# Kernel tuning notes

Hardware: AMD Instinct MI355X
Metric: run time of the kernel (lower is better)

The kernel has to match this reference:

```python
import jax, jax.numpy as jnp
import numpy as np

CH = 256
CQK = CH // 8
B, H, W = 4, 64, 64


def setup_inputs() -> dict:
    key = jax.random.key(0)
    ks = jax.random.split(key, 8)
    s_qk = 1.0 / np.sqrt(CH)  # MSR init for 1x1 conv: std = 1/sqrt(fan_in)
    x = jax.random.normal(ks[0], (B, CH, H, W), dtype=jnp.float32)
    Wq = jax.random.normal(ks[1], (CQK, CH), dtype=jnp.float32) * s_qk
    bq = jnp.zeros((CQK,), dtype=jnp.float32)
    Wk = jax.random.normal(ks[2], (CQK, CH), dtype=jnp.float32) * s_qk
    bk = jnp.zeros((CQK,), dtype=jnp.float32)
    Wv = jax.random.normal(ks[3], (CH, CH), dtype=jnp.float32) * s_qk
    bv = jnp.zeros((CH,), dtype=jnp.float32)
    # NOTE: module inits gamma=0; use a nonzero value so the attention branch is active
    gamma = jnp.float32(0.5) * jnp.ones((1,), dtype=jnp.float32)
    return {"x": x, "Wq": Wq, "bq": bq, "Wk": Wk, "bk": bk, "Wv": Wv, "bv": bv, "gamma": gamma}


def reference(x, Wq, bq, Wk, bk, Wv, bv, gamma):
    b, c, h, w = x.shape
    n = h * w
    xf = x.reshape(b, c, n)  # [B, C, N]
    # 1x1 convs are per-pixel channel projections
    q = jnp.einsum('oc,bcn->bon', Wq, xf) + bq[:, None]  # [B, C/8, N]
    k = jnp.einsum('oc,bcn->bon', Wk, xf) + bk[:, None]  # [B, C/8, N]
    v = jnp.einsum('oc,bcn->bon', Wv, xf) + bv[:, None]  # [B, C, N]
    # scores[b, i, j] = q[:, i] . k[:, j]  (no scaling, as in source)
    att = jax.nn.softmax(jnp.einsum('bci,bcj->bij', q, k), axis=-1)  # [B, N, N]
    out = jnp.einsum('bcj,bij->bci', v, att).reshape(b, c, h, w)
    return x + gamma[0] * out
```

## Files before the change

kernel.cpp:

```cpp
#include <hip/hip_runtime.h>
#include <hip/hip_bf16.h>

typedef unsigned short u16;
typedef __attribute__((ext_vector_type(8))) __bf16 bf16x8;
typedef __attribute__((ext_vector_type(8))) short s16x8;
typedef __attribute__((ext_vector_type(4))) float f32x4;
typedef __attribute__((ext_vector_type(16))) float f32x16;

#define MFMA16(a, b, c) __builtin_amdgcn_mfma_f32_16x16x32_bf16((a), (b), (c), 0, 0, 0)
#define MFMA32(a, b, c) __builtin_amdgcn_mfma_f32_32x32x16_bf16((a), (b), (c), 0, 0, 0)

#define BN 4
#define CH 256
#define CQK 32
#define NPIX 4096

__device__ __forceinline__ u16 f2bf(float f) {
    __hip_bfloat16 h = __float2bfloat16(f);
    return *reinterpret_cast<u16*>(&h);
}

__device__ __forceinline__ f32x16 zero16() {
    f32x16 z;
#pragma unroll
    for (int i = 0; i < 16; ++i) z[i] = 0.f;
    return z;
}

__device__ __forceinline__ int perm16(int k) {
    return (k & 3) | ((k & 4) << 1) | ((k & 8) >> 1);
}

__global__ void k_transpose(const float* __restrict__ x, u16* __restrict__ xt) {
    __shared__ float xs[64][65];
    int n0 = blockIdx.x * 64, c0 = blockIdx.y * 64, b = blockIdx.z;
    int t = threadIdx.x;
    const float* xp = x + ((size_t)(b * CH + c0)) * NPIX + n0;
#pragma unroll
    for (int it = 0; it < 16; ++it) {
        int idx = it * 256 + t;
        int cc = idx >> 6, nn = idx & 63;
        xs[cc][nn] = xp[(size_t)cc * NPIX + nn];
    }
    __syncthreads();
    u16* op = xt + ((size_t)(b * NPIX + n0)) * CH + c0;
#pragma unroll
    for (int it = 0; it < 16; ++it) {
        int idx = it * 256 + t;
        int nn = idx >> 6, cc = idx & 63;
        op[(size_t)nn * CH + cc] = f2bf(xs[cc][nn]);
    }
}

__global__ void k_wcvt(const float* __restrict__ Wq, const float* __restrict__ Wk,
                       const float* __restrict__ Wv, u16* __restrict__ Wbf) {
    int idx = blockIdx.x * 256 + threadIdx.x;
    int o = idx >> 8, c = idx & 255;
    float v;
    if (o < 32) v = Wq[o * 256 + c];
    else if (o < 64) v = Wk[(o - 32) * 256 + c];
    else v = Wv[(o - 64) * 256 + c];
    Wbf[idx] = f2bf(v);
}

__launch_bounds__(256, 1)
__global__ void k_proj(const u16* __restrict__ Wbf, const u16* __restrict__ xt,
                       const float* __restrict__ bq, const float* __restrict__ bk,
                       const float* __restrict__ bv,
                       u16* __restrict__ qb, u16* __restrict__ kb, u16* __restrict__ vb) {
    int b = blockIdx.y, n0 = blockIdx.x * 64;
    int t = threadIdx.x, w = t >> 6, l = t & 63;
    int lr = l & 15, lg = l >> 4;

    f32x4 acc[5][4];
#pragma unroll
    for (int s = 0; s < 5; ++s)
#pragma unroll
        for (int u = 0; u < 4; ++u) acc[s][u] = f32x4{0.f, 0.f, 0.f, 0.f};

    const u16* xtb = xt + ((size_t)(b * NPIX + n0)) * CH;

#pragma unroll
    for (int kk = 0; kk < 8; ++kk) {
        int kof = kk * 32 + lg * 8;
        bf16x8 af[5], bfr[4];
#pragma unroll
        for (int s = 0; s < 5; ++s) {
            int o = w * 16 + s * 64 + lr;
            af[s] = *reinterpret_cast<const bf16x8*>(Wbf + (size_t)o * 256 + kof);
        }
#pragma unroll
        for (int u = 0; u < 4; ++u) {
            int n = u * 16 + lr;
            bfr[u] = *reinterpret_cast<const bf16x8*>(xtb + (size_t)n * CH + kof);
        }
#pragma unroll
        for (int s = 0; s < 5; ++s)
#pragma unroll
            for (int u = 0; u < 4; ++u) acc[s][u] = MFMA16(af[s], bfr[u], acc[s][u]);
    }

    int lrp = perm16(lr);
#pragma unroll
    for (int s = 0; s < 5; ++s) {
        int o0 = w * 16 + s * 64;
#pragma unroll
        for (int r = 0; r < 4; ++r) {
            int o = o0 + lg * 4 + r;
            float bias = (o < 32) ? bq[o] : (o < 64) ? bk[o - 32] : bv[o - 64];
#pragma unroll
            for (int u = 0; u < 4; ++u) {
                float val = acc[s][u][r] + bias;
                u16 h = f2bf(val);
                if (o < 32) qb[((size_t)b * NPIX + n0 + u * 16 + lr) * CQK + o] = h;
                else if (o < 64) kb[((size_t)b * NPIX + n0 + u * 16 + lr) * CQK + (o - 32)] = h;
                else vb[((size_t)(b * CH + (o - 64))) * NPIX + n0 + u * 16 + lrp] = h;
            }
        }
    }
}

template <int NCHUNK>
__launch_bounds__(256, 2)
__global__ void k_attn2(const u16* __restrict__ qb, const u16* __restrict__ kb,
                        const u16* __restrict__ vb, const float* __restrict__ x,
                        const float* __restrict__ gamma,
                        float* __restrict__ pacc, float* __restrict__ plsum,
                        float* __restrict__ out) {
    constexpr int JCH = NPIX / NCHUNK;
    constexpr int NT = JCH / 32;
    int it = blockIdx.x, s = blockIdx.y, b = blockIdx.z;
    int t = threadIdx.x, w = t >> 6, l = t & 63;
    int lr = l & 31, hi = l >> 5;
    int i0 = it * 128;
    int j0 = s * JCH;

    __shared__ u16 vlds[2][256][40];
    __shared__ float lsl[128];

    const u16* qrow = qb + ((size_t)b * NPIX + i0 + w * 32 + lr) * CQK;
    bf16x8 qf0 = *(const bf16x8*)(qrow + hi * 8);
    bf16x8 qf1 = *(const bf16x8*)(qrow + 16 + hi * 8);

    const u16* kbase = kb + (size_t)b * NPIX * CQK;
    const u16* vbase = vb + (size_t)(b * CH) * NPIX;

    f32x16 acc[8];
#pragma unroll
    for (int ct = 0; ct < 8; ++ct) acc[ct] = zero16();
    float lsum_p = 0.f;

    int srow = t >> 2, swg = t & 3;

    bf16x8 vst[4];
#pragma unroll
    for (int m = 0; m < 4; ++m)
        vst[m] = *(const bf16x8*)(vbase + (size_t)(64 * m + srow) * NPIX + j0 + swg * 8);
#pragma unroll
    for (int m = 0; m < 4; ++m)
        *(bf16x8*)(&vlds[0][64 * m + srow][swg * 8]) = vst[m];
    __syncthreads();

    const u16* krow = kbase + (size_t)(j0 + lr) * CQK;
    bf16x8 kc0 = *(const bf16x8*)(krow + hi * 8);
    bf16x8 kc1 = *(const bf16x8*)(krow + 16 + hi * 8);

    for (int tt = 0; tt < NT; ++tt) {
        int cur = tt & 1;
        bool more = (tt + 1 < NT);
        int jn = j0 + (more ? (tt + 1) * 32 : 0);

        if (more) {
#pragma unroll
            for (int m = 0; m < 4; ++m)
                vst[m] = *(const bf16x8*)(vbase + (size_t)(64 * m + srow) * NPIX + jn + swg * 8);
        }
        const u16* krn = kbase + (size_t)(jn + lr) * CQK;
        bf16x8 kn0 = *(const bf16x8*)(krn + hi * 8);
        bf16x8 kn1 = *(const bf16x8*)(krn + 16 + hi * 8);

        f32x16 sf = MFMA32(kc0, qf0, zero16());
        sf = MFMA32(kc1, qf1, sf);

        float P[16];
#pragma unroll
        for (int r = 0; r < 16; ++r) {
            P[r] = __expf(sf[r] - 32.0f);
            lsum_p += P[r];
        }

        s16x8 w0, w1;
#pragma unroll
        for (int e = 0; e < 8; ++e) {
            w0[e] = (short)f2bf(P[e]);
            w1[e] = (short)f2bf(P[8 + e]);
        }
        bf16x8 pa0 = __builtin_bit_cast(bf16x8, w0);
        bf16x8 pa1 = __builtin_bit_cast(bf16x8, w1);

#pragma unroll
        for (int ct = 0; ct < 8; ++ct) {
            const u16* vr = &vlds[cur][ct * 32 + lr][hi * 8];
            bf16x8 vf0 = *(const bf16x8*)(vr);
            bf16x8 vf1 = *(const bf16x8*)(vr + 16);
            acc[ct] = MFMA32(pa0, vf0, acc[ct]);
            acc[ct] = MFMA32(pa1, vf1, acc[ct]);
        }
        kc0 = kn0; kc1 = kn1;

        __syncthreads();
        if (more) {
#pragma unroll
            for (int m = 0; m < 4; ++m)
                *(bf16x8*)(&vlds[cur ^ 1][64 * m + srow][swg * 8]) = vst[m];
        }
        __syncthreads();
    }

    lsum_p += __shfl_xor(lsum_p, 32);

    if constexpr (NCHUNK == 1) {
        float g = gamma[0];
        if (l < 32) lsl[w * 32 + l] = g / lsum_p;
        __syncthreads();
#pragma unroll
        for (int ct = 0; ct < 8; ++ct) {
            int c = ct * 32 + lr;
            const float* xp = x + ((size_t)(b * CH + c)) * NPIX + i0;
            float* op = out + ((size_t)(b * CH + c)) * NPIX + i0;
#pragma unroll
            for (int r = 0; r < 16; ++r) {
                int il = w * 32 + (r & 3) + 8 * (r >> 2) + 4 * hi;
                op[il] = xp[il] + acc[ct][r] * lsl[il];
            }
        }
    } else {
        size_t pbase = ((((size_t)s * BN + b) * 32 + it) * 256) * 128;
#pragma unroll
        for (int ct = 0; ct < 8; ++ct) {
            int c = ct * 32 + lr;
#pragma unroll
            for (int q = 0; q < 4; ++q) {
                int il0 = w * 32 + 8 * q + 4 * hi;
                f32x4 vv = {acc[ct][4 * q], acc[ct][4 * q + 1],
                            acc[ct][4 * q + 2], acc[ct][4 * q + 3]};
                *(f32x4*)(pacc + pbase + (size_t)c * 128 + il0) = vv;
            }
        }
        if (l < 32)
            plsum[(((size_t)s * BN + b) * 32 + it) * 128 + w * 32 + l] = lsum_p;
    }
}

template <int NCHUNK>
__global__ void k_reduce(const float* __restrict__ pacc, const float* __restrict__ plsum,
                         const float* __restrict__ x, const float* __restrict__ gamma,
                         float* __restrict__ out) {
    int cg = blockIdx.x, it = blockIdx.y, b = blockIdx.z;
    int t = threadIdx.x;
    int c0 = cg * 32;
    __shared__ float invl[128];

    if (t < 128) {
        float lt = 0.f;
#pragma unroll
        for (int s = 0; s < NCHUNK; ++s)
            lt += plsum[(((size_t)s * BN + b) * 32 + it) * 128 + t];
        invl[t] = gamma[0] / lt;
    }
    __syncthreads();

    const size_t chunk_stride = (size_t)BN * 32 * 256 * 128;
    size_t base = (((size_t)b * 32 + it) * 256 + c0) * 128;

#pragma unroll
    for (int k = 0; k < 4; ++k) {
        int v = k * 256 + t;
        int cl = v >> 5;
        int iv = (v & 31) * 4;
        size_t off = base + (size_t)cl * 128 + iv;
        f32x4 a = {0.f, 0.f, 0.f, 0.f};
#pragma unroll
        for (int s = 0; s < NCHUNK; ++s) {
            f32x4 p = *(const f32x4*)(pacc + (size_t)s * chunk_stride + off);
            a += p;
        }
        f32x4 il4 = *(const f32x4*)(&invl[iv]);
        size_t oi = ((size_t)(b * CH + c0 + cl)) * NPIX + it * 128 + iv;
        f32x4 xi = *(const f32x4*)(x + oi);
        f32x4 r = xi + a * il4;
        *(f32x4*)(out + oi) = r;
    }
}

extern "C" void kernel_launch(void* const* d_in, const int* in_sizes, int n_in,
                              void* d_out, int out_size, void* d_ws, size_t ws_size,
                              hipStream_t stream) {
    const float* x = (const float*)d_in[0];
    const float* Wq = (const float*)d_in[1];
    const float* bq = (const float*)d_in[2];
    const float* Wk = (const float*)d_in[3];
    const float* bk = (const float*)d_in[4];
    const float* Wv = (const float*)d_in[5];
    const float* bv = (const float*)d_in[6];
    const float* gamma = (const float*)d_in[7];
    float* out = (float*)d_out;

    char* ws = (char*)d_ws;
    u16* xt = (u16*)(ws);
    u16* Wbf = (u16*)(ws + 8388608);
    u16* qb = (u16*)(ws + 8388608 + 163840);
    u16* kb = (u16*)(ws + 8388608 + 163840 + 1048576);
    u16* vb = (u16*)(ws + 8388608 + 163840 + 2097152);
    const size_t base_end = 8388608 + 163840 + 2097152 + 8388608;
    float* pacc = (float*)(ws + base_end);

    hipLaunchKernelGGL(k_transpose, dim3(64, 4, 4), dim3(256), 0, stream, x, xt);
    hipLaunchKernelGGL(k_wcvt, dim3(320), dim3(256), 0, stream, Wq, Wk, Wv, Wbf);
    hipLaunchKernelGGL(k_proj, dim3(64, 4), dim3(256), 0, stream, Wbf, xt, bq, bk, bv, qb, kb, vb);

    const size_t pacc4 = (size_t)4 * BN * NPIX * CH * 4;
    const size_t pls4 = (size_t)4 * BN * NPIX * 4;
    const size_t pacc2 = pacc4 / 2, pls2 = pls4 / 2;

    if (ws_size >= base_end + pacc4 + pls4) {
        float* plsum = (float*)(ws + base_end + pacc4);
        hipLaunchKernelGGL(k_attn2<4>, dim3(32, 4, 4), dim3(256), 0, stream,
                           qb, kb, vb, x, gamma, pacc, plsum, out);
        hipLaunchKernelGGL(k_reduce<4>, dim3(8, 32, 4), dim3(256), 0, stream,
                           pacc, plsum, x, gamma, out);
    } else if (ws_size >= base_end + pacc2 + pls2) {
        float* plsum = (float*)(ws + base_end + pacc2);
        hipLaunchKernelGGL(k_attn2<2>, dim3(32, 2, 4), dim3(256), 0, stream,
                           qb, kb, vb, x, gamma, pacc, plsum, out);
        hipLaunchKernelGGL(k_reduce<2>, dim3(8, 32, 4), dim3(256), 0, stream,
                           pacc, plsum, x, gamma, out);
    } else {
        hipLaunchKernelGGL(k_attn2<1>, dim3(32, 1, 4), dim3(256), 0, stream,
                           qb, kb, vb, x, gamma, pacc, pacc, out);
    }
}
```

Baseline: 94.96 us.

## Software-pipeline QK softmax one tile ahead of PV with unrolled double buffer

Restructures the attention inner loop into a two-tile unrolled software pipeline. The QK score MFMAs and exp/bf16 conversion for tile t+1 are issued before the PV MFMAs of tile t, so the exp and convert work can overlap the matrix work. One of the two barriers per tile is removed, and the PV block is wrapped in s_setprio to favour MFMA issue. This raises register pressure from the extra P fragments and assumes NT is even.

```diff
diff --git a/kernel.cpp b/kernel.cpp
--- a/kernel.cpp
+++ b/kernel.cpp
@@ -151,70 +151,77 @@
     float lsum_p = 0.f;
 
     int srow = t >> 2, swg = t & 3;
-
     bf16x8 vst[4];
-#pragma unroll
-    for (int m = 0; m < 4; ++m)
-        vst[m] = *(const bf16x8*)(vbase + (size_t)(64 * m + srow) * NPIX + j0 + swg * 8);
-#pragma unroll
-    for (int m = 0; m < 4; ++m)
-        *(bf16x8*)(&vlds[0][64 * m + srow][swg * 8]) = vst[m];
-    __syncthreads();
-
-    const u16* krow = kbase + (size_t)(j0 + lr) * CQK;
-    bf16x8 kc0 = *(const bf16x8*)(krow + hi * 8);
-    bf16x8 kc1 = *(const bf16x8*)(krow + 16 + hi * 8);
-
-    for (int tt = 0; tt < NT; ++tt) {
-        int cur = tt & 1;
-        bool more = (tt + 1 < NT);
-        int jn = j0 + (more ? (tt + 1) * 32 : 0);
-
-        if (more) {
-#pragma unroll
-            for (int m = 0; m < 4; ++m)
-                vst[m] = *(const bf16x8*)(vbase + (size_t)(64 * m + srow) * NPIX + jn + swg * 8);
-        }
-        const u16* krn = kbase + (size_t)(jn + lr) * CQK;
-        bf16x8 kn0 = *(const bf16x8*)(krn + hi * 8);
-        bf16x8 kn1 = *(const bf16x8*)(krn + 16 + hi * 8);
-
+    bf16x8 kc0, kc1;
+
+    auto vload = [&](int jt) {
+#pragma unroll
+        for (int m = 0; m < 4; ++m)
+            vst[m] = *(const bf16x8*)(vbase + (size_t)(64 * m + srow) * NPIX +
+                                      j0 + jt * 32 + swg * 8);
+    };
+    auto vwrite = [&](int buf) {
+#pragma unroll
+        for (int m = 0; m < 4; ++m)
+            *(bf16x8*)(&vlds[buf][64 * m + srow][swg * 8]) = vst[m];
+    };
+    auto kload = [&](int jt) {
+        const u16* kr = kbase + (size_t)(j0 + jt * 32 + lr) * CQK;
+        kc0 = *(const bf16x8*)(kr + hi * 8);
+        kc1 = *(const bf16x8*)(kr + 16 + hi * 8);
+    };
+    auto qk_soft = [&](bf16x8& pa0, bf16x8& pa1) {
         f32x16 sf = MFMA32(kc0, qf0, zero16());
         sf = MFMA32(kc1, qf1, sf);
-
-        float P[16];
-#pragma unroll
-        for (int r = 0; r < 16; ++r) {
-            P[r] = __expf(sf[r] - 32.0f);
-            lsum_p += P[r];
-        }
-
         s16x8 w0, w1;
 #pragma unroll
         for (int e = 0; e < 8; ++e) {
-            w0[e] = (short)f2bf(P[e]);
-            w1[e] = (short)f2bf(P[8 + e]);
-        }
-        bf16x8 pa0 = __builtin_bit_cast(bf16x8, w0);
-        bf16x8 pa1 = __builtin_bit_cast(bf16x8, w1);
-
+            float p0 = __expf(sf[e] - 32.0f);
+            float p1 = __expf(sf[8 + e] - 32.0f);
+            lsum_p += p0 + p1;
+            w0[e] = (short)f2bf(p0);
+            w1[e] = (short)f2bf(p1);
+        }
+        pa0 = __builtin_bit_cast(bf16x8, w0);
+        pa1 = __builtin_bit_cast(bf16x8, w1);
+    };
+    auto pv = [&](int buf, bf16x8 pa0, bf16x8 pa1) {
+        __builtin_amdgcn_s_setprio(1);
 #pragma unroll
         for (int ct = 0; ct < 8; ++ct) {
-            const u16* vr = &vlds[cur][ct * 32 + lr][hi * 8];
+            const u16* vr = &vlds[buf][ct * 32 + lr][hi * 8];
             bf16x8 vf0 = *(const bf16x8*)(vr);
             bf16x8 vf1 = *(const bf16x8*)(vr + 16);
             acc[ct] = MFMA32(pa0, vf0, acc[ct]);
             acc[ct] = MFMA32(pa1, vf1, acc[ct]);
         }
-        kc0 = kn0; kc1 = kn1;
-
+        __builtin_amdgcn_s_setprio(0);
+    };
+
+    bf16x8 paA0, paA1, paB0, paB1;
+    vload(0);
+    vwrite(0);
+    kload(0);
+    vload(1);
+    __syncthreads();
+    qk_soft(paA0, paA1);
+    kload(1);
+
+    for (int tp = 0; tp < NT; tp += 2) {
+        bool m2 = (tp + 2 < NT);
+        bool m3 = (tp + 3 < NT);
         __syncthreads();
-        if (more) {
-#pragma unroll
-            for (int m = 0; m < 4; ++m)
-                *(bf16x8*)(&vlds[cur ^ 1][64 * m + srow][swg * 8]) = vst[m];
-        }
+        vwrite(1);
+        if (m2) vload(tp + 2);
+        qk_soft(paB0, paB1);
+        if (m2) kload(tp + 2);
+        pv(0, paA0, paA1);
         __syncthreads();
+        if (m2) vwrite(0);
+        if (m3) vload(tp + 3);
+        if (m2) qk_soft(paA0, paA1);
+        if (m3) kload(tp + 3);
+        pv(1, paB0, paB1);
     }
 
     lsum_p += __shfl_xor(lsum_p, 32);
```

Result: no change. 96.23 us (+1.3%).

## Load V fragments directly from global and halve query tile per block

Applied to the files above, without the earlier changes.

Replaces the LDS double-buffered V staging with per-lane direct global loads into registers, using a two-stage software pipeline of V and K fragments. Each block now covers 64 query rows, with waves split across two channel halves, which doubles the grid to 1024 blocks. Block IDs are remapped so that blocks sharing a batch and chunk land on the same XCD for L2 reuse. MFMA priority hints are also added. This removes both __syncthreads per tile and the LDS traffic, but V is now read twice as often from global/L2, the register footprint grows, and the partial-sum writes become scalar.

```diff
diff --git a/kernel.cpp b/kernel.cpp
--- a/kernel.cpp
+++ b/kernel.cpp
@@ -122,133 +122,125 @@
 
 template <int NCHUNK>
 __launch_bounds__(256, 2)
-__global__ void k_attn2(const u16* __restrict__ qb, const u16* __restrict__ kb,
+__global__ void k_attn3(const u16* __restrict__ qb, const u16* __restrict__ kb,
                         const u16* __restrict__ vb, const float* __restrict__ x,
                         const float* __restrict__ gamma,
                         float* __restrict__ pacc, float* __restrict__ plsum,
                         float* __restrict__ out) {
     constexpr int JCH = NPIX / NCHUNK;
     constexpr int NT = JCH / 32;
-    int it = blockIdx.x, s = blockIdx.y, b = blockIdx.z;
+    int bid = blockIdx.x;
+    int s, b, it;
+    if constexpr (NCHUNK == 4) {
+        int xcd = bid & 7, slot = bid >> 3;
+        int combo = xcd + 8 * (slot >> 6);
+        s = combo >> 2; b = combo & 3; it = slot & 63;
+    } else if constexpr (NCHUNK == 2) {
+        int combo = bid & 7;
+        s = combo >> 2; b = combo & 3; it = bid >> 3;
+    } else {
+        s = 0; b = bid & 3; it = bid >> 2;
+    }
     int t = threadIdx.x, w = t >> 6, l = t & 63;
     int lr = l & 31, hi = l >> 5;
-    int i0 = it * 128;
+    int iq = w >> 1, ch = w & 1;
+    int i0 = it * 64;
     int j0 = s * JCH;
 
-    __shared__ u16 vlds[2][256][40];
-    __shared__ float lsl[128];
-
-    const u16* qrow = qb + ((size_t)b * NPIX + i0 + w * 32 + lr) * CQK;
+    __shared__ float lsl[64];
+
+    const u16* qrow = qb + ((size_t)b * NPIX + i0 + iq * 32 + lr) * CQK;
     bf16x8 qf0 = *(const bf16x8*)(qrow + hi * 8);
     bf16x8 qf1 = *(const bf16x8*)(qrow + 16 + hi * 8);
 
     const u16* kbase = kb + (size_t)b * NPIX * CQK;
-    const u16* vbase = vb + (size_t)(b * CH) * NPIX;
-
-    f32x16 acc[8];
-#pragma unroll
-    for (int ct = 0; ct < 8; ++ct) acc[ct] = zero16();
+    const u16* vlane = vb + ((size_t)(b * CH + ch * 128 + lr)) * NPIX;
+
+    f32x16 acc[4];
+#pragma unroll
+    for (int ct = 0; ct < 4; ++ct) acc[ct] = zero16();
     float lsum_p = 0.f;
 
-    int srow = t >> 2, swg = t & 3;
-
-    bf16x8 vst[4];
-#pragma unroll
-    for (int m = 0; m < 4; ++m)
-        vst[m] = *(const bf16x8*)(vbase + (size_t)(64 * m + srow) * NPIX + j0 + swg * 8);
-#pragma unroll
-    for (int m = 0; m < 4; ++m)
-        *(bf16x8*)(&vlds[0][64 * m + srow][swg * 8]) = vst[m];
-    __syncthreads();
-
-    const u16* krow = kbase + (size_t)(j0 + lr) * CQK;
-    bf16x8 kc0 = *(const bf16x8*)(krow + hi * 8);
-    bf16x8 kc1 = *(const bf16x8*)(krow + 16 + hi * 8);
-
-    for (int tt = 0; tt < NT; ++tt) {
-        int cur = tt & 1;
-        bool more = (tt + 1 < NT);
-        int jn = j0 + (more ? (tt + 1) * 32 : 0);
-
-        if (more) {
-#pragma unroll
-            for (int m = 0; m < 4; ++m)
-                vst[m] = *(const bf16x8*)(vbase + (size_t)(64 * m + srow) * NPIX + jn + swg * 8);
-        }
-        const u16* krn = kbase + (size_t)(jn + lr) * CQK;
-        bf16x8 kn0 = *(const bf16x8*)(krn + hi * 8);
-        bf16x8 kn1 = *(const bf16x8*)(krn + 16 + hi * 8);
-
-        f32x16 sf = MFMA32(kc0, qf0, zero16());
-        sf = MFMA32(kc1, qf1, sf);
-
-        float P[16];
-#pragma unroll
-        for (int r = 0; r < 16; ++r) {
-            P[r] = __expf(sf[r] - 32.0f);
-            lsum_p += P[r];
-        }
-
+    bf16x8 vfA[8], vfB[8], kA0, kA1, kB0, kB1;
+
+    auto vload = [&](bf16x8 (&vf)[8], int tt) {
+        int jp = j0 + tt * 32 + hi * 8;
+#pragma unroll
+        for (int ct = 0; ct < 4; ++ct) {
+            const u16* vp = vlane + (size_t)ct * (32 * NPIX) + jp;
+            vf[2 * ct] = *(const bf16x8*)(vp);
+            vf[2 * ct + 1] = *(const bf16x8*)(vp + 16);
+        }
+    };
+    auto kload = [&](bf16x8& k0, bf16x8& k1, int tt) {
+        const u16* kr = kbase + (size_t)(j0 + tt * 32 + lr) * CQK;
+        k0 = *(const bf16x8*)(kr + hi * 8);
+        k1 = *(const bf16x8*)(kr + 16 + hi * 8);
+    };
+    auto step = [&](bf16x8 (&vf)[8], bf16x8 k0, bf16x8 k1) {
+        f32x16 sf = MFMA32(k0, qf0, zero16());
+        sf = MFMA32(k1, qf1, sf);
         s16x8 w0, w1;
 #pragma unroll
         for (int e = 0; e < 8; ++e) {
-            w0[e] = (short)f2bf(P[e]);
-            w1[e] = (short)f2bf(P[8 + e]);
+            float p0 = __expf(sf[e] - 32.0f);
+            float p1 = __expf(sf[8 + e] - 32.0f);
+            lsum_p += p0 + p1;
+            w0[e] = (short)f2bf(p0);
+            w1[e] = (short)f2bf(p1);
         }
         bf16x8 pa0 = __builtin_bit_cast(bf16x8, w0);
         bf16x8 pa1 = __builtin_bit_cast(bf16x8, w1);
-
-#pragma unroll
-        for (int ct = 0; ct < 8; ++ct) {
-            const u16* vr = &vlds[cur][ct * 32 + lr][hi * 8];
-            bf16x8 vf0 = *(const bf16x8*)(vr);
-            bf16x8 vf1 = *(const bf16x8*)(vr + 16);
-            acc[ct] = MFMA32(pa0, vf0, acc[ct]);
-            acc[ct] = MFMA32(pa1, vf1, acc[ct]);
-        }
-        kc0 = kn0; kc1 = kn1;
-
-        __syncthreads();
-        if (more) {
-#pragma unroll
-            for (int m = 0; m < 4; ++m)
-                *(bf16x8*)(&vlds[cur ^ 1][64 * m + srow][swg * 8]) = vst[m];
-        }
-        __syncthreads();
+        __builtin_amdgcn_s_setprio(1);
+#pragma unroll
+        for (int ct = 0; ct < 4; ++ct) {
+            acc[ct] = MFMA32(vf[2 * ct], pa0, acc[ct]);
+            acc[ct] = MFMA32(vf[2 * ct + 1], pa1, acc[ct]);
+        }
+        __builtin_amdgcn_s_setprio(0);
+    };
+
+    vload(vfA, 0);
+    kload(kA0, kA1, 0);
+    for (int tp = 0; tp < NT; tp += 2) {
+        int t1 = (tp + 1 < NT) ? tp + 1 : 0;
+        int t2 = (tp + 2 < NT) ? tp + 2 : 0;
+        vload(vfB, t1);
+        kload(kB0, kB1, t1);
+        step(vfA, kA0, kA1);
+        vload(vfA, t2);
+        kload(kA0, kA1, t2);
+        step(vfB, kB0, kB1);
     }
 
     lsum_p += __shfl_xor(lsum_p, 32);
 
     if constexpr (NCHUNK == 1) {
         float g = gamma[0];
-        if (l < 32) lsl[w * 32 + l] = g / lsum_p;
+        if (ch == 0 && l < 32) lsl[iq * 32 + l] = g / lsum_p;
         __syncthreads();
-#pragma unroll
-        for (int ct = 0; ct < 8; ++ct) {
-            int c = ct * 32 + lr;
-            const float* xp = x + ((size_t)(b * CH + c)) * NPIX + i0;
-            float* op = out + ((size_t)(b * CH + c)) * NPIX + i0;
+        float inv = lsl[iq * 32 + lr];
+#pragma unroll
+        for (int ct = 0; ct < 4; ++ct) {
 #pragma unroll
             for (int r = 0; r < 16; ++r) {
-                int il = w * 32 + (r & 3) + 8 * (r >> 2) + 4 * hi;
-                op[il] = xp[il] + acc[ct][r] * lsl[il];
+                int c = ch * 128 + ct * 32 + (r & 3) + 8 * (r >> 2) + 4 * hi;
+                size_t oi = ((size_t)(b * CH + c)) * NPIX + i0 + iq * 32 + lr;
+                out[oi] = x[oi] + acc[ct][r] * inv;
             }
         }
     } else {
-        size_t pbase = ((((size_t)s * BN + b) * 32 + it) * 256) * 128;
-#pragma unroll
-        for (int ct = 0; ct < 8; ++ct) {
-            int c = ct * 32 + lr;
-#pragma unroll
-            for (int q = 0; q < 4; ++q) {
-                int il0 = w * 32 + 8 * q + 4 * hi;
-                f32x4 vv = {acc[ct][4 * q], acc[ct][4 * q + 1],
-                            acc[ct][4 * q + 2], acc[ct][4 * q + 3]};
-                *(f32x4*)(pacc + pbase + (size_t)c * 128 + il0) = vv;
+        size_t pbase = (((size_t)s * BN + b) * 64 + it) * (256 * 64);
+#pragma unroll
+        for (int ct = 0; ct < 4; ++ct) {
+#pragma unroll
+            for (int r = 0; r < 16; ++r) {
+                int c = ch * 128 + ct * 32 + (r & 3) + 8 * (r >> 2) + 4 * hi;
+                pacc[pbase + (size_t)c * 64 + iq * 32 + lr] = acc[ct][r];
             }
         }
-        if (l < 32)
-            plsum[(((size_t)s * BN + b) * 32 + it) * 128 + w * 32 + l] = lsum_p;
+        if (ch == 0 && l < 32)
+            plsum[(((size_t)s * BN + b) * 64 + it) * 64 + iq * 32 + l] = lsum_p;
     }
 }
 
@@ -259,26 +251,26 @@
     int cg = blockIdx.x, it = blockIdx.y, b = blockIdx.z;
     int t = threadIdx.x;
     int c0 = cg * 32;
-    __shared__ float invl[128];
-
-    if (t < 128) {
+    __shared__ float invl[64];
+
+    if (t < 64) {
         float lt = 0.f;
 #pragma unroll
         for (int s = 0; s < NCHUNK; ++s)
-            lt += plsum[(((size_t)s * BN + b) * 32 + it) * 128 + t];
+            lt += plsum[(((size_t)s * BN + b) * 64 + it) * 64 + t];
         invl[t] = gamma[0] / lt;
     }
     __syncthreads();
 
-    const size_t chunk_stride = (size_t)BN * 32 * 256 * 128;
-    size_t base = (((size_t)b * 32 + it) * 256 + c0) * 128;
-
-#pragma unroll
-    for (int k = 0; k < 4; ++k) {
+    const size_t chunk_stride = (size_t)BN * 64 * 256 * 64;
+    size_t base = (((size_t)b * 64 + it) * 256 + c0) * 64;
+
+#pragma unroll
+    for (int k = 0; k < 2; ++k) {
         int v = k * 256 + t;
-        int cl = v >> 5;
-        int iv = (v & 31) * 4;
-        size_t off = base + (size_t)cl * 128 + iv;
+        int cl = v >> 4;
+        int iv = (v & 15) * 4;
+        size_t off = base + (size_t)cl * 64 + iv;
         f32x4 a = {0.f, 0.f, 0.f, 0.f};
 #pragma unroll
         for (int s = 0; s < NCHUNK; ++s) {
@@ -286,7 +278,7 @@
             a += p;
         }
         f32x4 il4 = *(const f32x4*)(&invl[iv]);
-        size_t oi = ((size_t)(b * CH + c0 + cl)) * NPIX + it * 128 + iv;
+        size_t oi = ((size_t)(b * CH + c0 + cl)) * NPIX + it * 64 + iv;
         f32x4 xi = *(const f32x4*)(x + oi);
         f32x4 r = xi + a * il4;
         *(f32x4*)(out + oi) = r;
@@ -325,18 +317,18 @@
 
     if (ws_size >= base_end + pacc4 + pls4) {
         float* plsum = (float*)(ws + base_end + pacc4);
-        hipLaunchKernelGGL(k_attn2<4>, dim3(32, 4, 4), dim3(256), 0, stream,
+        hipLaunchKernelGGL(k_attn3<4>, dim3(1024), dim3(256), 0, stream,
                            qb, kb, vb, x, gamma, pacc, plsum, out);
-        hipLaunchKernelGGL(k_reduce<4>, dim3(8, 32, 4), dim3(256), 0, stream,
+        hipLaunchKernelGGL(k_reduce<4>, dim3(8, 64, 4), dim3(256), 0, stream,
                            pacc, plsum, x, gamma, out);
     } else if (ws_size >= base_end + pacc2 + pls2) {
         float* plsum = (float*)(ws + base_end + pacc2);
-        hipLaunchKernelGGL(k_attn2<2>, dim3(32, 2, 4), dim3(256), 0, stream,
+        hipLaunchKernelGGL(k_attn3<2>, dim3(512), dim3(256), 0, stream,
                            qb, kb, vb, x, gamma, pacc, plsum, out);
-        hipLaunchKernelGGL(k_reduce<2>, dim3(8, 32, 4), dim3(256), 0, stream,
+        hipLaunchKernelGGL(k_reduce<2>, dim3(8, 64, 4), dim3(256), 0, stream,
                            pacc, plsum, x, gamma, out);
     } else {
-        hipLaunchKernelGGL(k_attn2<1>, dim3(32, 1, 4), dim3(256), 0, stream,
+        hipLaunchKernelGGL(k_attn3<1>, dim3(256), dim3(256), 0, stream,
                            qb, kb, vb, x, gamma, pacc, pacc, out);
     }
 }
```

After: 181.6 us. 91.2% more time.

## Retile attention waves as 2x2 query/channel split, 64-wide key steps, bf16 partials

Applied to the files above, without the earlier changes.

Each wave now covers 64 query rows and half the 256 output channels, instead of 32 query rows and all channels. Each V fragment read from LDS then feeds two query subtiles, and each K-tile step processes 64 keys with a double-buffered V tile. V prefetch is issued two steps ahead, and the PV MFMAs run at raised wave priority. Split-chunk partial accumulators are stored and reduced as bf16 rather than fp32, halving partial traffic at some cost in precision, and QK^T/exp is now computed twice as often across waves.

```diff
diff --git a/kernel.cpp b/kernel.cpp
--- a/kernel.cpp
+++ b/kernel.cpp
@@ -3,9 +3,11 @@
 
 typedef unsigned short u16;
 typedef __attribute__((ext_vector_type(8))) __bf16 bf16x8;
-typedef __attribute__((ext_vector_type(8))) short s16x8;
+typedef __attribute__((ext_vector_type(8))) unsigned short u16x8;
 typedef __attribute__((ext_vector_type(4))) float f32x4;
 typedef __attribute__((ext_vector_type(16))) float f32x16;
+typedef __attribute__((ext_vector_type(4))) unsigned int u32x4;
+typedef __attribute__((ext_vector_type(2))) unsigned int u32x2;
 
 #define MFMA16(a, b, c) __builtin_amdgcn_mfma_f32_16x16x32_bf16((a), (b), (c), 0, 0, 0)
 #define MFMA32(a, b, c) __builtin_amdgcn_mfma_f32_32x32x16_bf16((a), (b), (c), 0, 0, 0)
@@ -18,6 +20,14 @@
 __device__ __forceinline__ u16 f2bf(float f) {
     __hip_bfloat16 h = __float2bfloat16(f);
     return *reinterpret_cast<u16*>(&h);
+}
+
+__device__ __forceinline__ unsigned pack2(float a, float b) {
+    return (unsigned)f2bf(a) | ((unsigned)f2bf(b) << 16);
+}
+
+__device__ __forceinline__ float bf2f(u16 v) {
+    return __uint_as_float(((unsigned)v) << 16);
 }
 
 __device__ __forceinline__ f32x16 zero16() {
@@ -122,138 +132,167 @@
 
 template <int NCHUNK>
 __launch_bounds__(256, 2)
-__global__ void k_attn2(const u16* __restrict__ qb, const u16* __restrict__ kb,
+__global__ void k_attn4(const u16* __restrict__ qb, const u16* __restrict__ kb,
                         const u16* __restrict__ vb, const float* __restrict__ x,
                         const float* __restrict__ gamma,
-                        float* __restrict__ pacc, float* __restrict__ plsum,
+                        u16* __restrict__ pacc, float* __restrict__ plsum,
                         float* __restrict__ out) {
     constexpr int JCH = NPIX / NCHUNK;
-    constexpr int NT = JCH / 32;
+    constexpr int NT = JCH / 64;
     int it = blockIdx.x, s = blockIdx.y, b = blockIdx.z;
     int t = threadIdx.x, w = t >> 6, l = t & 63;
     int lr = l & 31, hi = l >> 5;
+    int iqw = w >> 1, ch = w & 1;
     int i0 = it * 128;
     int j0 = s * JCH;
 
-    __shared__ u16 vlds[2][256][40];
+    __shared__ u16 vlds[2][256][72];
     __shared__ float lsl[128];
 
-    const u16* qrow = qb + ((size_t)b * NPIX + i0 + w * 32 + lr) * CQK;
-    bf16x8 qf0 = *(const bf16x8*)(qrow + hi * 8);
-    bf16x8 qf1 = *(const bf16x8*)(qrow + 16 + hi * 8);
+    bf16x8 qf[2][2];
+#pragma unroll
+    for (int is = 0; is < 2; ++is) {
+        const u16* qrow = qb + ((size_t)b * NPIX + i0 + iqw * 64 + is * 32 + lr) * CQK;
+        qf[is][0] = *(const bf16x8*)(qrow + hi * 8);
+        qf[is][1] = *(const bf16x8*)(qrow + 16 + hi * 8);
+    }
 
     const u16* kbase = kb + (size_t)b * NPIX * CQK;
     const u16* vbase = vb + (size_t)(b * CH) * NPIX;
 
-    f32x16 acc[8];
-#pragma unroll
-    for (int ct = 0; ct < 8; ++ct) acc[ct] = zero16();
-    float lsum_p = 0.f;
-
-    int srow = t >> 2, swg = t & 3;
-
-    bf16x8 vst[4];
-#pragma unroll
-    for (int m = 0; m < 4; ++m)
-        vst[m] = *(const bf16x8*)(vbase + (size_t)(64 * m + srow) * NPIX + j0 + swg * 8);
-#pragma unroll
-    for (int m = 0; m < 4; ++m)
-        *(bf16x8*)(&vlds[0][64 * m + srow][swg * 8]) = vst[m];
+    f32x16 acc[2][4];
+#pragma unroll
+    for (int is = 0; is < 2; ++is)
+#pragma unroll
+        for (int ct = 0; ct < 4; ++ct) acc[is][ct] = zero16();
+    float lsum[2] = {0.f, 0.f};
+
+    int srow = t >> 2, sslot = t & 3;
+    bf16x8 vst[8];
+    bf16x8 kc[4];
+
+    auto vload = [&](int tt) {
+#pragma unroll
+        for (int e = 0; e < 8; ++e)
+            vst[e] = *(const bf16x8*)(vbase + (size_t)(64 * (e >> 1) + srow) * NPIX +
+                                      j0 + tt * 64 + (e & 1) * 32 + sslot * 8);
+    };
+    auto vwrite = [&](int buf) {
+#pragma unroll
+        for (int e = 0; e < 8; ++e)
+            *(bf16x8*)(&vlds[buf][64 * (e >> 1) + srow][(e & 1) * 32 + sslot * 8]) = vst[e];
+    };
+    auto kload = [&](int tt) {
+#pragma unroll
+        for (int sub = 0; sub < 2; ++sub) {
+            const u16* kr = kbase + (size_t)(j0 + tt * 64 + sub * 32 + lr) * CQK;
+            kc[2 * sub] = *(const bf16x8*)(kr + hi * 8);
+            kc[2 * sub + 1] = *(const bf16x8*)(kr + 16 + hi * 8);
+        }
+    };
+    auto qksoft = [&](int sub, bf16x8 (&pa)[4]) {
+#pragma unroll
+        for (int is = 0; is < 2; ++is) {
+            f32x16 sf = MFMA32(kc[2 * sub], qf[is][0], zero16());
+            sf = MFMA32(kc[2 * sub + 1], qf[is][1], sf);
+            float P[16];
+#pragma unroll
+            for (int e = 0; e < 16; ++e) {
+                P[e] = __expf(sf[e] - 32.0f);
+                lsum[is] += P[e];
+            }
+            u32x4 w0 = {pack2(P[0], P[1]), pack2(P[2], P[3]),
+                        pack2(P[4], P[5]), pack2(P[6], P[7])};
+            u32x4 w1 = {pack2(P[8], P[9]), pack2(P[10], P[11]),
+                        pack2(P[12], P[13]), pack2(P[14], P[15])};
+            pa[is * 2] = __builtin_bit_cast(bf16x8, w0);
+            pa[is * 2 + 1] = __builtin_bit_cast(bf16x8, w1);
+        }
+    };
+    auto pv = [&](int sub, int buf, bf16x8 (&pa)[4]) {
+        __builtin_amdgcn_s_setprio(1);
+#pragma unroll
+        for (int ct = 0; ct < 4; ++ct) {
+            const u16* vr = &vlds[buf][ch * 128 + ct * 32 + lr][sub * 32 + hi * 8];
+            bf16x8 vf0 = *(const bf16x8*)(vr);
+            bf16x8 vf1 = *(const bf16x8*)(vr + 16);
+#pragma unroll
+            for (int is = 0; is < 2; ++is) {
+                acc[is][ct] = MFMA32(pa[is * 2], vf0, acc[is][ct]);
+                acc[is][ct] = MFMA32(pa[is * 2 + 1], vf1, acc[is][ct]);
+            }
+        }
+        __builtin_amdgcn_s_setprio(0);
+    };
+
+    vload(0);
+    kload(0);
+    vwrite(0);
+    vload(1);
     __syncthreads();
-
-    const u16* krow = kbase + (size_t)(j0 + lr) * CQK;
-    bf16x8 kc0 = *(const bf16x8*)(krow + hi * 8);
-    bf16x8 kc1 = *(const bf16x8*)(krow + 16 + hi * 8);
 
     for (int tt = 0; tt < NT; ++tt) {
         int cur = tt & 1;
-        bool more = (tt + 1 < NT);
-        int jn = j0 + (more ? (tt + 1) * 32 : 0);
-
-        if (more) {
-#pragma unroll
-            for (int m = 0; m < 4; ++m)
-                vst[m] = *(const bf16x8*)(vbase + (size_t)(64 * m + srow) * NPIX + jn + swg * 8);
-        }
-        const u16* krn = kbase + (size_t)(jn + lr) * CQK;
-        bf16x8 kn0 = *(const bf16x8*)(krn + hi * 8);
-        bf16x8 kn1 = *(const bf16x8*)(krn + 16 + hi * 8);
-
-        f32x16 sf = MFMA32(kc0, qf0, zero16());
-        sf = MFMA32(kc1, qf1, sf);
-
-        float P[16];
-#pragma unroll
-        for (int r = 0; r < 16; ++r) {
-            P[r] = __expf(sf[r] - 32.0f);
-            lsum_p += P[r];
-        }
-
-        s16x8 w0, w1;
-#pragma unroll
-        for (int e = 0; e < 8; ++e) {
-            w0[e] = (short)f2bf(P[e]);
-            w1[e] = (short)f2bf(P[8 + e]);
-        }
-        bf16x8 pa0 = __builtin_bit_cast(bf16x8, w0);
-        bf16x8 pa1 = __builtin_bit_cast(bf16x8, w1);
-
-#pragma unroll
-        for (int ct = 0; ct < 8; ++ct) {
-            const u16* vr = &vlds[cur][ct * 32 + lr][hi * 8];
-            bf16x8 vf0 = *(const bf16x8*)(vr);
-            bf16x8 vf1 = *(const bf16x8*)(vr + 16);
-            acc[ct] = MFMA32(pa0, vf0, acc[ct]);
-            acc[ct] = MFMA32(pa1, vf1, acc[ct]);
-        }
-        kc0 = kn0; kc1 = kn1;
-
+        bf16x8 pa[4];
+        qksoft(0, pa);
+        pv(0, cur, pa);
+        qksoft(1, pa);
+        if (tt + 1 < NT) kload(tt + 1);
+        pv(1, cur, pa);
         __syncthreads();
-        if (more) {
-#pragma unroll
-            for (int m = 0; m < 4; ++m)
-                *(bf16x8*)(&vlds[cur ^ 1][64 * m + srow][swg * 8]) = vst[m];
-        }
+        vwrite(cur ^ 1);
+        if (tt + 2 < NT) vload(tt + 2);
         __syncthreads();
     }
 
-    lsum_p += __shfl_xor(lsum_p, 32);
+    lsum[0] += __shfl_xor(lsum[0], 32);
+    lsum[1] += __shfl_xor(lsum[1], 32);
 
     if constexpr (NCHUNK == 1) {
         float g = gamma[0];
-        if (l < 32) lsl[w * 32 + l] = g / lsum_p;
+        if (ch == 0 && l < 32) {
+            lsl[iqw * 64 + l] = g / lsum[0];
+            lsl[iqw * 64 + 32 + l] = g / lsum[1];
+        }
         __syncthreads();
 #pragma unroll
-        for (int ct = 0; ct < 8; ++ct) {
-            int c = ct * 32 + lr;
-            const float* xp = x + ((size_t)(b * CH + c)) * NPIX + i0;
-            float* op = out + ((size_t)(b * CH + c)) * NPIX + i0;
-#pragma unroll
-            for (int r = 0; r < 16; ++r) {
-                int il = w * 32 + (r & 3) + 8 * (r >> 2) + 4 * hi;
-                op[il] = xp[il] + acc[ct][r] * lsl[il];
-            }
-        }
+        for (int is = 0; is < 2; ++is)
+#pragma unroll
+            for (int ct = 0; ct < 4; ++ct) {
+                int c = ch * 128 + ct * 32 + lr;
+                const float* xp = x + ((size_t)(b * CH + c)) * NPIX + i0;
+                float* op = out + ((size_t)(b * CH + c)) * NPIX + i0;
+#pragma unroll
+                for (int r = 0; r < 16; ++r) {
+                    int il = iqw * 64 + is * 32 + (r & 3) + 8 * (r >> 2) + 4 * hi;
+                    op[il] = xp[il] + acc[is][ct][r] * lsl[il];
+                }
+            }
     } else {
         size_t pbase = ((((size_t)s * BN + b) * 32 + it) * 256) * 128;
 #pragma unroll
-        for (int ct = 0; ct < 8; ++ct) {
-            int c = ct * 32 + lr;
-#pragma unroll
-            for (int q = 0; q < 4; ++q) {
-                int il0 = w * 32 + 8 * q + 4 * hi;
-                f32x4 vv = {acc[ct][4 * q], acc[ct][4 * q + 1],
-                            acc[ct][4 * q + 2], acc[ct][4 * q + 3]};
-                *(f32x4*)(pacc + pbase + (size_t)c * 128 + il0) = vv;
-            }
-        }
-        if (l < 32)
-            plsum[(((size_t)s * BN + b) * 32 + it) * 128 + w * 32 + l] = lsum_p;
+        for (int is = 0; is < 2; ++is)
+#pragma unroll
+            for (int ct = 0; ct < 4; ++ct) {
+                int c = ch * 128 + ct * 32 + lr;
+#pragma unroll
+                for (int q = 0; q < 4; ++q) {
+                    int il0 = iqw * 64 + is * 32 + 8 * q + 4 * hi;
+                    u32x2 pr = {pack2(acc[is][ct][4 * q], acc[is][ct][4 * q + 1]),
+                                pack2(acc[is][ct][4 * q + 2], acc[is][ct][4 * q + 3])};
+                    *(u32x2*)(pacc + pbase + (size_t)c * 128 + il0) = pr;
+                }
+            }
+        if (ch == 0 && l < 32) {
+            size_t lb = (((size_t)s * BN + b) * 32 + it) * 128 + iqw * 64;
+            plsum[lb + l] = lsum[0];
+            plsum[lb + 32 + l] = lsum[1];
+        }
     }
 }
 
 template <int NCHUNK>
-__global__ void k_reduce(const float* __restrict__ pacc, const float* __restrict__ plsum,
+__global__ void k_reduce(const u16* __restrict__ pacc, const float* __restrict__ plsum,
                          const float* __restrict__ x, const float* __restrict__ gamma,
                          float* __restrict__ out) {
     int cg = blockIdx.x, it = blockIdx.y, b = blockIdx.z;
@@ -274,22 +313,25 @@
     size_t base = (((size_t)b * 32 + it) * 256 + c0) * 128;
 
 #pragma unroll
-    for (int k = 0; k < 4; ++k) {
+    for (int k = 0; k < 2; ++k) {
         int v = k * 256 + t;
-        int cl = v >> 5;
-        int iv = (v & 31) * 4;
-        size_t off = base + (size_t)cl * 128 + iv;
-        f32x4 a = {0.f, 0.f, 0.f, 0.f};
+        int cl = v >> 4;
+        int io = (v & 15) * 8;
+        size_t off = base + (size_t)cl * 128 + io;
+        f32x4 a0 = {0.f, 0.f, 0.f, 0.f}, a1 = a0;
 #pragma unroll
         for (int s = 0; s < NCHUNK; ++s) {
-            f32x4 p = *(const f32x4*)(pacc + (size_t)s * chunk_stride + off);
-            a += p;
-        }
-        f32x4 il4 = *(const f32x4*)(&invl[iv]);
-        size_t oi = ((size_t)(b * CH + c0 + cl)) * NPIX + it * 128 + iv;
-        f32x4 xi = *(const f32x4*)(x + oi);
-        f32x4 r = xi + a * il4;
-        *(f32x4*)(out + oi) = r;
+            u16x8 p = *(const u16x8*)(pacc + (size_t)s * chunk_stride + off);
+            a0[0] += bf2f(p[0]); a0[1] += bf2f(p[1]); a0[2] += bf2f(p[2]); a0[3] += bf2f(p[3]);
+            a1[0] += bf2f(p[4]); a1[1] += bf2f(p[5]); a1[2] += bf2f(p[6]); a1[3] += bf2f(p[7]);
+        }
+        f32x4 i0v = *(const f32x4*)(&invl[io]);
+        f32x4 i1v = *(const f32x4*)(&invl[io + 4]);
+        size_t oi = ((size_t)(b * CH + c0 + cl)) * NPIX + it * 128 + io;
+        f32x4 x0 = *(const f32x4*)(x + oi);
+        f32x4 x1 = *(const f32x4*)(x + oi + 4);
+        *(f32x4*)(out + oi) = x0 + a0 * i0v;
+        *(f32x4*)(out + oi + 4) = x1 + a1 * i1v;
     }
 }
 
@@ -313,30 +355,30 @@
     u16* kb = (u16*)(ws + 8388608 + 163840 + 1048576);
     u16* vb = (u16*)(ws + 8388608 + 163840 + 2097152);
     const size_t base_end = 8388608 + 163840 + 2097152 + 8388608;
-    float* pacc = (float*)(ws + base_end);
+    u16* pacc = (u16*)(ws + base_end);
 
     hipLaunchKernelGGL(k_transpose, dim3(64, 4, 4), dim3(256), 0, stream, x, xt);
     hipLaunchKernelGGL(k_wcvt, dim3(320), dim3(256), 0, stream, Wq, Wk, Wv, Wbf);
     hipLaunchKernelGGL(k_proj, dim3(64, 4), dim3(256), 0, stream, Wbf, xt, bq, bk, bv, qb, kb, vb);
 
-    const size_t pacc4 = (size_t)4 * BN * NPIX * CH * 4;
+    const size_t pacc4 = (size_t)4 * BN * NPIX * CH * 2;
     const size_t pls4 = (size_t)4 * BN * NPIX * 4;
     const size_t pacc2 = pacc4 / 2, pls2 = pls4 / 2;
 
     if (ws_size >= base_end + pacc4 + pls4) {
         float* plsum = (float*)(ws + base_end + pacc4);
-        hipLaunchKernelGGL(k_attn2<4>, dim3(32, 4, 4), dim3(256), 0, stream,
+        hipLaunchKernelGGL(k_attn4<4>, dim3(32, 4, 4), dim3(256), 0, stream,
                            qb, kb, vb, x, gamma, pacc, plsum, out);
         hipLaunchKernelGGL(k_reduce<4>, dim3(8, 32, 4), dim3(256), 0, stream,
                            pacc, plsum, x, gamma, out);
     } else if (ws_size >= base_end + pacc2 + pls2) {
         float* plsum = (float*)(ws + base_end + pacc2);
-        hipLaunchKernelGGL(k_attn2<2>, dim3(32, 2, 4), dim3(256), 0, stream,
+        hipLaunchKernelGGL(k_attn4<2>, dim3(32, 2, 4), dim3(256), 0, stream,
                            qb, kb, vb, x, gamma, pacc, plsum, out);
         hipLaunchKernelGGL(k_reduce<2>, dim3(8, 32, 4), dim3(256), 0, stream,
                            pacc, plsum, x, gamma, out);
     } else {
-        hipLaunchKernelGGL(k_attn2<1>, dim3(32, 1, 4), dim3(256), 0, stream,
-                           qb, kb, vb, x, gamma, pacc, pacc, out);
-    }
-}
+        hipLaunchKernelGGL(k_attn4<1>, dim3(32, 1, 4), dim3(256), 0, stream,
+                           qb, kb, vb, x, gamma, pacc, (float*)pacc, out);
+    }
+}
```

Result: slower. 106.0 us (+11.6%).
